# Optimization experiments

Measured on AMD Instinct MI355X. Metric: run time of the kernel, lower is better.

Reference implementation:

```python
import jax, jax.numpy as jnp
import numpy as np
from jax import lax

B, T, D, L, OUT, HORIZON, TSLOTS, NDAY = 512, 24, 1024, 2, 325, 12, 288, 7


def setup_inputs() -> dict:
    key = jax.random.key(0)
    ks = jax.random.split(key, 20)
    s_d = 1.0 / np.sqrt(D)
    s_o = 1.0 / np.sqrt(OUT)
    inp = {
        'data': jax.random.normal(ks[0], (B, T, OUT), jnp.float32),
        'time': jax.random.randint(ks[1], (B, T), 0, TSLOTS),
        'weekday': jax.random.randint(ks[2], (B,), 0, NDAY),
        # embedding params
        'w_data': jax.random.normal(ks[3], (OUT, D), jnp.float32) * s_o,
        'b_data': jnp.zeros((D,), jnp.float32),
        'time_table': jax.random.normal(ks[4], (TSLOTS, D), jnp.float32) * 0.02,
        'day_table': jax.random.normal(ks[5], (NDAY, D), jnp.float32) * 0.02,
        # encoder GRU (input_size == hidden_size == D for all layers)
        'enc_Wih': jax.random.uniform(ks[6], (L, 3 * D, D), jnp.float32, -s_d, s_d),
        'enc_Whh': jax.random.uniform(ks[7], (L, 3 * D, D), jnp.float32, -s_d, s_d),
        'enc_bih': jax.random.uniform(ks[8], (L, 3 * D), jnp.float32, -s_d, s_d),
        'enc_bhh': jax.random.uniform(ks[9], (L, 3 * D), jnp.float32, -s_d, s_d),
        # decoder GRU
        'dec_Wih': jax.random.uniform(ks[10], (L, 3 * D, D), jnp.float32, -s_d, s_d),
        'dec_Whh': jax.random.uniform(ks[11], (L, 3 * D, D), jnp.float32, -s_d, s_d),
        'dec_bih': jax.random.uniform(ks[12], (L, 3 * D), jnp.float32, -s_d, s_d),
        'dec_bhh': jax.random.uniform(ks[13], (L, 3 * D), jnp.float32, -s_d, s_d),
        # decoder output MLP (dropout=0 -> linear)
        'w_mlp': jax.random.uniform(ks[14], (D, OUT), jnp.float32, -s_d, s_d),
        'b_mlp': jnp.zeros((OUT,), jnp.float32),
    }
    return inp


def _gru_cell(h, x, Wih, Whh, bih, bhh):
    # torch GRUCell math. h,x: [B,D]
    gx = x @ Wih.T + bih            # [B,3D]
    gh = h @ Whh.T + bhh
    xr, xz, xn = jnp.split(gx, 3, axis=-1)
    hr, hz, hn = jnp.split(gh, 3, axis=-1)
    r = jax.nn.sigmoid(xr + hr)
    z = jax.nn.sigmoid(xz + hz)
    n = jnp.tanh(xn + r * hn)
    return (1.0 - z) * n + z * h


def _gru_layer(x, h0, Wih, Whh, bih, bhh):
    # x: [B,S,D] -> outputs [B,S,D], final h [B,D]
    def step(h, xt):
        h2 = _gru_cell(h, xt, Wih, Whh, bih, bhh)
        return h2, h2
    hT, ys = lax.scan(step, h0, jnp.moveaxis(x, 1, 0))
    return jnp.moveaxis(ys, 0, 1), hT


def reference(data, time, weekday, w_data, b_data, time_table, day_table,
              enc_Wih, enc_Whh, enc_bih, enc_bhh,
              dec_Wih, dec_Whh, dec_bih, dec_bhh, w_mlp, b_mlp):
    def embed(d, t, wd):  # d:[B,S,OUT] t:[B,S] wd:[B]
        return (d @ w_data + b_data
                + time_table[t % TSLOTS]
                + day_table[wd][:, None, :])

    # ---- encoder over history (all but last step) ----
    x = embed(data[:, :-1], time[:, :-1], weekday)  # [B,T-1,D]
    h_layers = []
    for l in range(L):
        x, hl = _gru_layer(x, jnp.zeros((B, D), x.dtype),
                           enc_Wih[l], enc_Whh[l], enc_bih[l], enc_bhh[l])
        h_layers.append(hl)
    hidden = jnp.stack(h_layers)  # [L,B,D]

    def dec_step(carry, _):
        hidden, data_i, time_i = carry  # [L,B,D], [B,1,OUT], [B,1]
        xi = embed(data_i, time_i, weekday)[:, 0]  # [B,D]
        new_h = []
        h_in = xi
        for l in range(L):
            hl = _gru_cell(hidden[l], h_in, dec_Wih[l], dec_Whh[l],
                           dec_bih[l], dec_bhh[l])
            new_h.append(hl)
            h_in = hl
        res = h_in @ w_mlp + b_mlp              # [B,OUT]
        out_i = data_i[:, 0] + res
        data_next = data_i[:, 0] + lax.stop_gradient(res)
        return (jnp.stack(new_h), data_next[:, None], time_i + 1), out_i

    carry0 = (hidden, data[:, -1:], time[:, -1:])
    _, outs = lax.scan(dec_step, carry0, None, length=HORIZON)  # [H,B,OUT]
    return jnp.moveaxis(outs, 0, 1)  # [B,H,OUT]
```

## Files before the change

### kernel.cpp

```cpp
#include <hip/hip_runtime.h>
#include <math.h>

#define B_ 512
#define T_ 24
#define TM1 23
#define D_ 1024
#define OUT_ 325
#define HORIZON_ 12

typedef unsigned short ushort_t;
typedef __attribute__((ext_vector_type(8))) short bf16x8;
typedef __attribute__((ext_vector_type(4))) float f32x4;

#define MFMA16(a, b, c) __builtin_amdgcn_mfma_f32_16x16x32_bf16((a), (b), (c), 0, 0, 0)

__device__ __forceinline__ ushort_t f2b(float f) {
  union { float f; unsigned u; } v; v.f = f;
  unsigned r = (v.u + 0x7fffu + ((v.u >> 16) & 1u)) >> 16;
  return (ushort_t)r;
}
__device__ __forceinline__ float b2f(ushort_t s) {
  union { unsigned u; float f; } v; v.u = ((unsigned)s) << 16;
  return v.f;
}

__device__ __forceinline__ size_t pidx16(int m, int k, int K) {
  return (((size_t)(m >> 4) * (K >> 5) + (k >> 5)) * 64
          + ((m & 15) + (((k >> 3) & 3) << 4))) * 8 + (k & 7);
}

#define GLOAD16(src, dst) \
  __builtin_amdgcn_global_load_lds((const __attribute__((address_space(1))) void*)(src), \
                                   (__attribute__((address_space(3))) void*)(dst), 16, 0, 0)

#define WAITV2() asm volatile("s_waitcnt vmcnt(2)" ::: "memory")
#define WAITV4() asm volatile("s_waitcnt vmcnt(4)" ::: "memory")
#define WAITV0() asm volatile("s_waitcnt vmcnt(0)" ::: "memory")
#define BARRIER_() { __builtin_amdgcn_s_barrier(); __builtin_amdgcn_sched_barrier(0); }

__global__ __launch_bounds__(256) void enc_diag(
    int k,
    const ushort_t* __restrict__ Hp0, const float* __restrict__ Hf0,
    float* __restrict__ Hf0o, ushort_t* __restrict__ Hp0o,
    const ushort_t* __restrict__ Whh0, const float* __restrict__ bhh0,
    const ushort_t* __restrict__ GXbuf, ushort_t* __restrict__ Y0p,
    const ushort_t* __restrict__ Hp1, const float* __restrict__ Hf1,
    float* __restrict__ Hf1o, ushort_t* __restrict__ Hp1o,
    const ushort_t* __restrict__ Wih1, const ushort_t* __restrict__ Whh1,
    const float* __restrict__ bih1, const float* __restrict__ bhh1)
{
  __shared__ ushort_t lds[3][16 * 512];
  const int tid = threadIdx.x, lane = tid & 63, w = tid >> 6;
  const int bid = blockIdx.x;
  const int z = bid >> 9, bx = (bid >> 5) & 15, by = bid & 31;
  const int wm = w >> 1, wn = w & 1;
  const int d = by * 32 + wn * 16 + (lane & 15);

  if (z == 0) {
    if (k >= TM1) return;
    const ushort_t* GXslot = GXbuf + (size_t)k * 512 * 3072;
    ushort_t* Seqp = Y0p + (size_t)k * 512 * 1024;
    f32x4 acc[3] = {};
    auto stage = [&](int buf, int kb) {
      #pragma unroll
      for (int r = 0; r < 2; ++r) {
        int s = w * 2 + r;
        const ushort_t* src;
        if (s < 2) src = Hp0 + ((size_t)(((bx * 32 + s * 16) >> 4) * 32 + kb)) * 512 + lane * 8;
        else { int g = (s - 2) >> 1, hf = (s - 2) & 1;
          src = Whh0 + ((size_t)((g * 64 + by * 2 + hf) * 32 + kb)) * 512 + lane * 8; }
        GLOAD16(src, &lds[buf][s * 512 + lane * 8]);
      }
    };
    stage(0, 0); stage(1, 1);
    for (int kb = 0; kb < 32; ++kb) {
      if (kb < 31) { WAITV2(); } else { WAITV0(); }
      BARRIER_();
      if (kb + 2 < 32) stage((kb + 2) % 3, kb + 2);
      const ushort_t* L = lds[kb % 3];
      bf16x8 a = *(const bf16x8*)(L + wm * 512 + lane * 8);
      #pragma unroll
      for (int g = 0; g < 3; ++g) {
        bf16x8 b = *(const bf16x8*)(L + (2 + g * 2 + wn) * 512 + lane * 8);
        acc[g] = MFMA16(a, b, acc[g]);
      }
    }
    const float bh_r = bhh0[d], bh_z = bhh0[D_ + d], bh_n = bhh0[2 * D_ + d];
    #pragma unroll
    for (int q = 0; q < 4; ++q) {
      int m = bx * 32 + wm * 16 + ((lane >> 4) << 2) + q;
      const ushort_t* gxp = GXslot + (size_t)m * 3072 + d;
      float gx_r = b2f(gxp[0]), gx_z = b2f(gxp[D_]), gx_n = b2f(gxp[2 * D_]);
      float rr = 1.f / (1.f + __expf(-(gx_r + acc[0][q] + bh_r)));
      float zz = 1.f / (1.f + __expf(-(gx_z + acc[1][q] + bh_z)));
      float nn = tanhf(gx_n + rr * (acc[2][q] + bh_n));
      float h = Hf0[(size_t)m * D_ + d];
      float hnew = (1.f - zz) * nn + zz * h;
      Hf0o[(size_t)m * D_ + d] = hnew;
      ushort_t hb = f2b(hnew);
      size_t pi = pidx16(m, d, D_);
      Hp0o[pi] = hb; Seqp[pi] = hb;
    }
  } else {
    if (k < 1) return;
    const ushort_t* Xp_ = Y0p + (size_t)(k - 1) * 512 * 1024;
    f32x4 accx[3] = {}, acch[3] = {};
    auto stage = [&](int buf, int kb) {
      #pragma unroll
      for (int r = 0; r < 4; ++r) {
        int s = w * 4 + r;
        const ushort_t* src;
        if (s < 2) src = Xp_ + ((size_t)(((bx * 32 + s * 16) >> 4) * 32 + kb)) * 512 + lane * 8;
        else if (s < 4) src = Hp1 + ((size_t)(((bx * 32 + (s - 2) * 16) >> 4) * 32 + kb)) * 512 + lane * 8;
        else if (s < 10) { int g = (s - 4) >> 1, hf = (s - 4) & 1;
          src = Wih1 + ((size_t)((g * 64 + by * 2 + hf) * 32 + kb)) * 512 + lane * 8; }
        else { int g = (s - 10) >> 1, hf = (s - 10) & 1;
          src = Whh1 + ((size_t)((g * 64 + by * 2 + hf) * 32 + kb)) * 512 + lane * 8; }
        GLOAD16(src, &lds[buf][s * 512 + lane * 8]);
      }
    };
    stage(0, 0); stage(1, 1);
    for (int kb = 0; kb < 32; ++kb) {
      if (kb < 31) { WAITV4(); } else { WAITV0(); }
      BARRIER_();
      if (kb + 2 < 32) stage((kb + 2) % 3, kb + 2);
      const ushort_t* L = lds[kb % 3];
      bf16x8 ax = *(const bf16x8*)(L + (0 + wm) * 512 + lane * 8);
      bf16x8 ah = *(const bf16x8*)(L + (2 + wm) * 512 + lane * 8);
      #pragma unroll
      for (int g = 0; g < 3; ++g) {
        bf16x8 bxw = *(const bf16x8*)(L + (4 + g * 2 + wn) * 512 + lane * 8);
        bf16x8 bhw = *(const bf16x8*)(L + (10 + g * 2 + wn) * 512 + lane * 8);
        accx[g] = MFMA16(ax, bxw, accx[g]);
        acch[g] = MFMA16(ah, bhw, acch[g]);
      }
    }
    const float bi_r = bih1[d], bi_z = bih1[D_ + d], bi_n = bih1[2 * D_ + d];
    const float bh_r = bhh1[d], bh_z = bhh1[D_ + d], bh_n = bhh1[2 * D_ + d];
    #pragma unroll
    for (int q = 0; q < 4; ++q) {
      int m = bx * 32 + wm * 16 + ((lane >> 4) << 2) + q;
      float rr = 1.f / (1.f + __expf(-(accx[0][q] + bi_r + acch[0][q] + bh_r)));
      float zz = 1.f / (1.f + __expf(-(accx[1][q] + bi_z + acch[1][q] + bh_z)));
      float nn = tanhf(accx[2][q] + bi_n + rr * (acch[2][q] + bh_n));
      float h = Hf1[(size_t)m * D_ + d];
      float hnew = (1.f - zz) * nn + zz * h;
      Hf1o[(size_t)m * D_ + d] = hnew;
      Hp1o[pidx16(m, d, D_)] = f2b(hnew);
    }
  }
}

__global__ __launch_bounds__(256) void dec_cell0(
    const ushort_t* __restrict__ DCp, const ushort_t* __restrict__ Hp,
    const float* __restrict__ Hf,
    const ushort_t* __restrict__ W0dp, const ushort_t* __restrict__ Whh0,
    const float* __restrict__ bhh0,
    const float* __restrict__ CTt, const float* __restrict__ CBd,
    const int* __restrict__ timev, int step,
    float* __restrict__ Hf_out, ushort_t* __restrict__ Hp_out)
{
  __shared__ ushort_t lds[3][8 * 512];
  const int tid = threadIdx.x, lane = tid & 63, w = tid >> 6;
  const int bid = blockIdx.x;
  const int bx = bid >> 5, by = bid & 31;
  const int wm = w >> 1, wn = w & 1;
  const int d = by * 32 + wn * 16 + (lane & 15);
  f32x4 accx[3] = {}, acch[3] = {};
  const int NT = 43;

  auto stage = [&](int buf, int j) {
    #pragma unroll
    for (int r = 0; r < 2; ++r) {
      int s = w * 2 + r;
      const ushort_t* src;
      if (j < 32) {
        if (s < 2) src = Hp + ((size_t)(((bx * 32 + s * 16) >> 4) * 32 + j)) * 512 + lane * 8;
        else { int g = (s - 2) >> 1, hf = (s - 2) & 1;
          src = Whh0 + ((size_t)((g * 64 + by * 2 + hf) * 32 + j)) * 512 + lane * 8; }
      } else {
        int jj = j - 32;
        if (s < 2) src = DCp + ((size_t)(((bx * 32 + s * 16) >> 4) * 11 + jj)) * 512 + lane * 8;
        else { int g = (s - 2) >> 1, hf = (s - 2) & 1;
          src = W0dp + ((size_t)((g * 64 + by * 2 + hf) * 11 + jj)) * 512 + lane * 8; }
      }
      GLOAD16(src, &lds[buf][s * 512 + lane * 8]);
    }
  };

  stage(0, 0); stage(1, 1);
  for (int j = 0; j < NT; ++j) {
    if (j < NT - 1) { WAITV2(); } else { WAITV0(); }
    BARRIER_();
    if (j + 2 < NT) stage((j + 2) % 3, j + 2);
    const ushort_t* L = lds[j % 3];
    bf16x8 a = *(const bf16x8*)(L + wm * 512 + lane * 8);
    if (j < 32) {
      #pragma unroll
      for (int g = 0; g < 3; ++g) {
        bf16x8 b = *(const bf16x8*)(L + (2 + g * 2 + wn) * 512 + lane * 8);
        acch[g] = MFMA16(a, b, acch[g]);
      }
    } else {
      #pragma unroll
      for (int g = 0; g < 3; ++g) {
        bf16x8 b = *(const bf16x8*)(L + (2 + g * 2 + wn) * 512 + lane * 8);
        accx[g] = MFMA16(a, b, accx[g]);
      }
    }
  }

  const float bh_r = bhh0[d], bh_z = bhh0[D_ + d], bh_n = bhh0[2 * D_ + d];
  #pragma unroll
  for (int q = 0; q < 4; ++q) {
    int m = bx * 32 + wm * 16 + ((lane >> 4) << 2) + q;
    int ti = (timev[m * T_ + (T_ - 1)] + step) % 288;
    const float* ctt = CTt + (size_t)ti * 3072;
    const float* cb  = CBd + (size_t)m * 3072;
    float gx_r = accx[0][q] + ctt[d] + cb[d];
    float gx_z = accx[1][q] + ctt[D_ + d] + cb[D_ + d];
    float gx_n = accx[2][q] + ctt[2 * D_ + d] + cb[2 * D_ + d];
    float rr = 1.f / (1.f + __expf(-(gx_r + acch[0][q] + bh_r)));
    float zz = 1.f / (1.f + __expf(-(gx_z + acch[1][q] + bh_z)));
    float nn = tanhf(gx_n + rr * (acch[2][q] + bh_n));
    float h = Hf[(size_t)m * D_ + d];
    float hnew = (1.f - zz) * nn + zz * h;
    Hf_out[(size_t)m * D_ + d] = hnew;
    Hp_out[pidx16(m, d, D_)] = f2b(hnew);
  }
}

__global__ __launch_bounds__(256) void gru_cell32(
    const ushort_t* __restrict__ Xp_, const ushort_t* __restrict__ Hp,
    const float* __restrict__ Hf,
    const ushort_t* __restrict__ Wih_l, const ushort_t* __restrict__ Whh_l,
    const float* __restrict__ bih_l, const float* __restrict__ bhh_l,
    float* __restrict__ Hf_out, ushort_t* __restrict__ Hp_out)
{
  __shared__ ushort_t lds[3][16 * 512];
  const int tid = threadIdx.x, lane = tid & 63, w = tid >> 6;
  const int bid = blockIdx.x;
  const int bx = bid >> 5, by = bid & 31;
  const int wm = w >> 1, wn = w & 1;
  const int d = by * 32 + wn * 16 + (lane & 15);
  f32x4 accx[3] = {}, acch[3] = {};

  auto stage = [&](int buf, int kb) {
    #pragma unroll
    for (int r = 0; r < 4; ++r) {
      int s = w * 4 + r;
      const ushort_t* src;
      if (s < 2) src = Xp_ + ((size_t)(((bx * 32 + s * 16) >> 4) * 32 + kb)) * 512 + lane * 8;
      else if (s < 4) src = Hp + ((size_t)(((bx * 32 + (s - 2) * 16) >> 4) * 32 + kb)) * 512 + lane * 8;
      else if (s < 10) { int g = (s - 4) >> 1, hf = (s - 4) & 1;
        src = Wih_l + ((size_t)((g * 64 + by * 2 + hf) * 32 + kb)) * 512 + lane * 8; }
      else { int g = (s - 10) >> 1, hf = (s - 10) & 1;
        src = Whh_l + ((size_t)((g * 64 + by * 2 + hf) * 32 + kb)) * 512 + lane * 8; }
      GLOAD16(src, &lds[buf][s * 512 + lane * 8]);
    }
  };

  stage(0, 0); stage(1, 1);
  for (int kb = 0; kb < 32; ++kb) {
    if (kb < 31) { WAITV4(); } else { WAITV0(); }
    BARRIER_();
    if (kb + 2 < 32) stage((kb + 2) % 3, kb + 2);
    const ushort_t* L = lds[kb % 3];
    bf16x8 ax = *(const bf16x8*)(L + (0 + wm) * 512 + lane * 8);
    bf16x8 ah = *(const bf16x8*)(L + (2 + wm) * 512 + lane * 8);
    #pragma unroll
    for (int g = 0; g < 3; ++g) {
      bf16x8 bxw = *(const bf16x8*)(L + (4 + g * 2 + wn) * 512 + lane * 8);
      bf16x8 bhw = *(const bf16x8*)(L + (10 + g * 2 + wn) * 512 + lane * 8);
      accx[g] = MFMA16(ax, bxw, accx[g]);
      acch[g] = MFMA16(ah, bhw, acch[g]);
    }
  }

  const float bi_r = bih_l[d], bi_z = bih_l[D_ + d], bi_n = bih_l[2 * D_ + d];
  const float bh_r = bhh_l[d], bh_z = bhh_l[D_ + d], bh_n = bhh_l[2 * D_ + d];
  #pragma unroll
  for (int q = 0; q < 4; ++q) {
    int m = bx * 32 + wm * 16 + ((lane >> 4) << 2) + q;
    float rr = 1.f / (1.f + __expf(-(accx[0][q] + bi_r + acch[0][q] + bh_r)));
    float zz = 1.f / (1.f + __expf(-(accx[1][q] + bi_z + acch[1][q] + bh_z)));
    float nn = tanhf(accx[2][q] + bi_n + rr * (acch[2][q] + bh_n));
    float h = Hf[(size_t)m * D_ + d];
    float hnew = (1.f - zz) * nn + zz * h;
    Hf_out[(size_t)m * D_ + d] = hnew;
    Hp_out[pidx16(m, d, D_)] = f2b(hnew);
  }
}

__global__ __launch_bounds__(256) void gemm_gx0_enc(
    const ushort_t* __restrict__ Ap, const ushort_t* __restrict__ W0p,
    const float* __restrict__ CTt, const float* __restrict__ CBe,
    const int* __restrict__ timev,
    ushort_t* __restrict__ GX)
{
  __shared__ ushort_t lds[2][16 * 512];
  const int tid = threadIdx.x, lane = tid & 63, w = tid >> 6;
  const int bx = blockIdx.x, by = blockIdx.y;
  const int wm = w >> 1, wn = w & 1;
  f32x4 acc[4][4] = {};

  auto stage = [&](int buf, int kb) {
    #pragma unroll
    for (int r = 0; r < 4; ++r) {
      int s = r * 4 + w;
      const ushort_t* src = (s < 8)
          ? Ap  + ((size_t)((bx * 8 + s) * 11 + kb)) * 512 + lane * 8
          : W0p + ((size_t)((by * 8 + (s - 8)) * 11 + kb)) * 512 + lane * 8;
      GLOAD16(src, &lds[buf][s * 512 + lane * 8]);
    }
  };

  stage(0, 0); __syncthreads();
  int cur = 0;
  for (int kb = 0; kb < 11; ++kb) {
    if (kb + 1 < 11) stage(cur ^ 1, kb + 1);
    const ushort_t* L = lds[cur];
    bf16x8 af[4], bf[4];
    #pragma unroll
    for (int f = 0; f < 4; ++f) {
      af[f] = *(const bf16x8*)(L + (wm * 4 + f) * 512 + lane * 8);
      bf[f] = *(const bf16x8*)(L + (8 + wn * 4 + f) * 512 + lane * 8);
    }
    #pragma unroll
    for (int fm = 0; fm < 4; ++fm)
      #pragma unroll
      for (int fn = 0; fn < 4; ++fn)
        acc[fm][fn] = MFMA16(af[fm], bf[fn], acc[fm][fn]);
    __syncthreads(); cur ^= 1;
  }

  float* fl = (float*)&lds[0][0];
  for (int fm = 0; fm < 4; ++fm) {
    #pragma unroll
    for (int q = 0; q < 4; ++q)
      #pragma unroll
      for (int fn = 0; fn < 4; ++fn)
        fl[(wm * 16 + ((lane >> 4) << 2) + q) * 132 + wn * 64 + fn * 16 + (lane & 15)]
            = acc[fm][fn][q];
    __syncthreads();
    #pragma unroll
    for (int it = 0; it < 2; ++it) {
      int idx = it * 256 + tid;
      int ml = idx >> 4, n0 = (idx & 15) * 8;
      int m = bx * 128 + (ml >> 4) * 64 + fm * 16 + (ml & 15);
      int b = m / 23, t = m - b * 23;
      int ti = timev[b * T_ + t] % 288;
      const float* ctt = CTt + (size_t)ti * 3072 + by * 128 + n0;
      const float* cb  = CBe + (size_t)b * 3072 + by * 128 + n0;
      const float* fr  = fl + ml * 132 + n0;
      bf16x8 o;
      #pragma unroll
      for (int j = 0; j < 8; ++j) o[j] = f2b(fr[j] + ctt[j] + cb[j]);
      *(bf16x8*)(GX + ((size_t)t * 512 + b) * 3072 + by * 128 + n0) = o;
    }
    __syncthreads();
  }
}

template<int EPI>
__global__ __launch_bounds__(256) void gemm64(
    const ushort_t* __restrict__ Ap, const ushort_t* __restrict__ Wp, int K32,
    const float* __restrict__ bias, int step,
    ushort_t* __restrict__ outp, float* __restrict__ outf,
    float* __restrict__ dout, ushort_t* __restrict__ DCp)
{
  __shared__ ushort_t lds[2][8 * 512];
  const int tid = threadIdx.x, lane = tid & 63, w = tid >> 6;
  const int bx = blockIdx.x, by = blockIdx.y;
  const int wm = w >> 1, wn = w & 1;
  f32x4 acc[2][2] = {};

  auto stage = [&](int buf, int kb) {
    #pragma unroll
    for (int r = 0; r < 2; ++r) {
      int s = r * 4 + w;
      const ushort_t* src = (s < 4)
          ? Ap + ((size_t)((bx * 4 + s) * K32 + kb)) * 512 + lane * 8
          : Wp + ((size_t)((by * 4 + (s - 4)) * K32 + kb)) * 512 + lane * 8;
      GLOAD16(src, &lds[buf][s * 512 + lane * 8]);
    }
  };

  stage(0, 0); __syncthreads();
  int cur = 0;
  for (int kb = 0; kb < K32; ++kb) {
    if (kb + 1 < K32) stage(cur ^ 1, kb + 1);
    const ushort_t* L = lds[cur];
    bf16x8 af[2], bf[2];
    #pragma unroll
    for (int f = 0; f < 2; ++f) {
      af[f] = *(const bf16x8*)(L + (wm * 2 + f) * 512 + lane * 8);
      bf[f] = *(const bf16x8*)(L + (4 + wn * 2 + f) * 512 + lane * 8);
    }
    #pragma unroll
    for (int fm = 0; fm < 2; ++fm)
      #pragma unroll
      for (int fn = 0; fn < 2; ++fn)
        acc[fm][fn] = MFMA16(af[fm], bf[fn], acc[fm][fn]);
    __syncthreads(); cur ^= 1;
  }

  #pragma unroll
  for (int fm = 0; fm < 2; ++fm) {
    #pragma unroll
    for (int q = 0; q < 4; ++q) {
      int m = bx * 64 + wm * 32 + fm * 16 + ((lane >> 4) << 2) + q;
      #pragma unroll
      for (int fn = 0; fn < 2; ++fn) {
        int n = by * 64 + wn * 32 + fn * 16 + (lane & 15);
        float v = acc[fm][fn][q];
        if (EPI == 0) {
          if (n < 352) outp[pidx16(m, n, 352)] = f2b(v);
        } else if (EPI == 1) {
          outf[(size_t)m * 3072 + n] = v;
        } else {
          if (n < OUT_) {
            v += bias[n] + outf[(size_t)m * OUT_ + n];
            dout[((size_t)m * HORIZON_ + step) * OUT_ + n] = v;
            outf[(size_t)m * OUT_ + n] = v;
            DCp[pidx16(m, n, 352)] = f2b(v);
          }
        }
      }
    }
  }
}

__global__ void build_cb(const float* __restrict__ CT, const float* __restrict__ bih0,
                         const int* __restrict__ weekday, float* __restrict__ CB)
{
  int idx = blockIdx.x * 256 + threadIdx.x;
  if (idx >= 512 * 3072) return;
  int b = idx / 3072, n = idx - b * 3072;
  CB[idx] = CT[(size_t)(288 + weekday[b]) * 3072 + n] + CT[(size_t)295 * 3072 + n] + bih0[n];
}

__global__ void pack_k1024(const float* __restrict__ src, ushort_t* __restrict__ dst,
                           int total, int Mvalid) {
  int stride = gridDim.x * 256;
  for (int i = blockIdx.x * 256 + threadIdx.x; i < total; i += stride) {
    int seg = i >> 6, q = i & 63;
    int m = (seg >> 5) * 16 + (q & 15);
    int k = (seg & 31) * 32 + (q >> 4) * 8;
    bf16x8 o;
    if (m < Mvalid) {
      const float* s = src + (size_t)m * 1024 + k;
      float4 v0 = *(const float4*)s, v1 = *(const float4*)(s + 4);
      o[0] = f2b(v0.x); o[1] = f2b(v0.y); o[2] = f2b(v0.z); o[3] = f2b(v0.w);
      o[4] = f2b(v1.x); o[5] = f2b(v1.y); o[6] = f2b(v1.z); o[7] = f2b(v1.w);
    } else o = bf16x8{0,0,0,0,0,0,0,0};
    *(bf16x8*)(dst + (size_t)i * 8) = o;
  }
}
__global__ void pack_wm(const float* __restrict__ w_mlp, ushort_t* __restrict__ dst) {
  int stride = gridDim.x * 256;
  for (int i = blockIdx.x * 256 + threadIdx.x; i < 384 * 128; i += stride) {
    int seg = i >> 6, q = i & 63;
    int n = (seg >> 5) * 16 + (q & 15);
    int k = (seg & 31) * 32 + (q >> 4) * 8;
    bf16x8 o;
    #pragma unroll
    for (int j = 0; j < 8; ++j)
      o[j] = (n < OUT_) ? f2b(w_mlp[(size_t)(k + j) * OUT_ + n]) : (short)0;
    *(bf16x8*)(dst + (size_t)i * 8) = o;
  }
}
__global__ void pack_ct(const float* __restrict__ time_table, const float* __restrict__ day_table,
                        const float* __restrict__ b_data, ushort_t* __restrict__ dst) {
  int stride = gridDim.x * 256;
  for (int i = blockIdx.x * 256 + threadIdx.x; i < 320 * 128; i += stride) {
    int seg = i >> 6, q = i & 63;
    int r = (seg >> 5) * 16 + (q & 15);
    int k = (seg & 31) * 32 + (q >> 4) * 8;
    const float* s = nullptr;
    if (r < 288) s = time_table + (size_t)r * 1024 + k;
    else if (r < 295) s = day_table + (size_t)(r - 288) * 1024 + k;
    else if (r == 295) s = b_data + k;
    bf16x8 o;
    #pragma unroll
    for (int j = 0; j < 8; ++j) o[j] = s ? f2b(s[j]) : (short)0;
    *(bf16x8*)(dst + (size_t)i * 8) = o;
  }
}
__global__ void pack_ae(const float* __restrict__ data, ushort_t* __restrict__ Ap) {
  int stride = gridDim.x * 256;
  const int total = (11776 / 16) * 11 * 64;
  for (int i = blockIdx.x * 256 + threadIdx.x; i < total; i += stride) {
    int seg = i >> 6, q = i & 63;
    int m = (seg / 11) * 16 + (q & 15);
    int k = (seg % 11) * 32 + (q >> 4) * 8;
    int b = m / TM1, t = m - b * TM1;
    const float* s = data + ((size_t)b * T_ + t) * OUT_;
    bf16x8 o;
    #pragma unroll
    for (int j = 0; j < 8; ++j) {
      int kk = k + j;
      o[j] = (kk < OUT_) ? f2b(s[kk]) : (short)0;
    }
    *(bf16x8*)(Ap + (size_t)i * 8) = o;
  }
}
__global__ void pack_dc(const float* __restrict__ data, ushort_t* __restrict__ DCp,
                        float* __restrict__ DC) {
  int stride = gridDim.x * 256;
  const int total = (512 / 16) * 11 * 64;
  for (int i = blockIdx.x * 256 + threadIdx.x; i < total; i += stride) {
    int seg = i >> 6, q = i & 63;
    int b = (seg / 11) * 16 + (q & 15);
    int k = (seg % 11) * 32 + (q >> 4) * 8;
    const float* s = data + ((size_t)b * T_ + (T_ - 1)) * OUT_;
    bf16x8 o;
    #pragma unroll
    for (int j = 0; j < 8; ++j) {
      int kk = k + j;
      float v = (kk < OUT_) ? s[kk] : 0.f;
      o[j] = f2b(v);
      if (kk < OUT_) DC[(size_t)b * OUT_ + kk] = v;
    }
    *(bf16x8*)(DCp + (size_t)i * 8) = o;
  }
}

extern "C" void kernel_launch(void* const* d_in, const int* in_sizes, int n_in,
                              void* d_out, int out_size, void* d_ws, size_t ws_size,
                              hipStream_t stream) {
  const float* data       = (const float*)d_in[0];
  const int*   timev      = (const int*)  d_in[1];
  const int*   weekday    = (const int*)  d_in[2];
  const float* w_data     = (const float*)d_in[3];
  const float* b_data     = (const float*)d_in[4];
  const float* time_table = (const float*)d_in[5];
  const float* day_table  = (const float*)d_in[6];
  const float* enc_Wih    = (const float*)d_in[7];
  const float* enc_Whh    = (const float*)d_in[8];
  const float* enc_bih    = (const float*)d_in[9];
  const float* enc_bhh    = (const float*)d_in[10];
  const float* dec_Wih    = (const float*)d_in[11];
  const float* dec_Whh    = (const float*)d_in[12];
  const float* dec_bih    = (const float*)d_in[13];
  const float* dec_bhh    = (const float*)d_in[14];
  const float* w_mlp      = (const float*)d_in[15];
  const float* b_mlp      = (const float*)d_in[16];
  float* out = (float*)d_out;

  char* base = (char*)d_ws;
  size_t o = 0;
  auto take = [&](size_t bytes) { void* p = base + o; o = (o + bytes + 511) & ~(size_t)511; return p; };
  const size_t WSZ = (size_t)6144 * 1024 * 2;
  ushort_t* Wih_e = (ushort_t*)take(WSZ);
  ushort_t* Whh_e = (ushort_t*)take(WSZ);
  ushort_t* Wih_d = (ushort_t*)take(WSZ);
  ushort_t* Whh_d = (ushort_t*)take(WSZ);
  ushort_t* WdTk  = (ushort_t*)take((size_t)384 * 1024 * 2);
  ushort_t* WmT   = (ushort_t*)take((size_t)384 * 1024 * 2);
  ushort_t* CTpk  = (ushort_t*)take((size_t)320 * 1024 * 2);
  ushort_t* W0ep  = (ushort_t*)take((size_t)3072 * 352 * 2);
  ushort_t* W0dp  = (ushort_t*)take((size_t)3072 * 352 * 2);
  float*    CTe   = (float*)take((size_t)320 * 3072 * 4);
  float*    CTd   = (float*)take((size_t)320 * 3072 * 4);
  float*    CBe   = (float*)take((size_t)512 * 3072 * 4);
  float*    CBd   = (float*)take((size_t)512 * 3072 * 4);
  ushort_t* Ap    = (ushort_t*)take((size_t)11776 * 352 * 2);
  ushort_t* Xp    = (ushort_t*)take((size_t)23 * 512 * 1024 * 2);
  ushort_t* GXbuf = (ushort_t*)take((size_t)23 * 512 * 3072 * 2);
  ushort_t* DCp   = (ushort_t*)take((size_t)512 * 352 * 2);
  float*    DC    = (float*)take((size_t)512 * OUT_ * 4);
  float*    Hfb   = (float*)take((size_t)4 * 512 * 1024 * 4 + (size_t)4 * 512 * 1024 * 2);
  if (o > ws_size) return;

  float* Hf0[2], *Hf1[2]; ushort_t* Hp0[2], *Hp1[2];
  ushort_t* Hpb = (ushort_t*)(Hfb + (size_t)4 * 512 * 1024);
  for (int p = 0; p < 2; ++p) {
    Hf0[p] = Hfb + (size_t)p * 512 * 1024;
    Hf1[p] = Hfb + (size_t)(2 + p) * 512 * 1024;
    Hp0[p] = Hpb + (size_t)p * 512 * 1024;
    Hp1[p] = Hpb + (size_t)(2 + p) * 512 * 1024;
  }

  const size_t WLAYER = (size_t)3072 * 1024;

  pack_k1024<<<3072, 256, 0, stream>>>(enc_Wih, Wih_e, 6144 * 128, 6144);
  pack_k1024<<<3072, 256, 0, stream>>>(enc_Whh, Whh_e, 6144 * 128, 6144);
  pack_k1024<<<3072, 256, 0, stream>>>(dec_Wih, Wih_d, 6144 * 128, 6144);
  pack_k1024<<<3072, 256, 0, stream>>>(dec_Whh, Whh_d, 6144 * 128, 6144);
  pack_k1024<<<192, 256, 0, stream>>>(w_data, WdTk, 384 * 128, OUT_);
  pack_wm<<<192, 256, 0, stream>>>(w_mlp, WmT);
  pack_ct<<<160, 256, 0, stream>>>(time_table, day_table, b_data, CTpk);
  pack_ae<<<2048, 256, 0, stream>>>(data, Ap);
  pack_dc<<<88, 256, 0, stream>>>(data, DCp, DC);

  gemm64<0><<<dim3(48, 6), 256, 0, stream>>>(Wih_e, WdTk, 32, nullptr, 0, W0ep, nullptr, nullptr, nullptr);
  gemm64<0><<<dim3(48, 6), 256, 0, stream>>>(Wih_d, WdTk, 32, nullptr, 0, W0dp, nullptr, nullptr, nullptr);
  gemm64<1><<<dim3(5, 48), 256, 0, stream>>>(CTpk, Wih_e, 32, nullptr, 0, nullptr, CTe, nullptr, nullptr);
  gemm64<1><<<dim3(5, 48), 256, 0, stream>>>(CTpk, Wih_d, 32, nullptr, 0, nullptr, CTd, nullptr, nullptr);
  build_cb<<<6144, 256, 0, stream>>>(CTe, enc_bih, weekday, CBe);
  build_cb<<<6144, 256, 0, stream>>>(CTd, dec_bih, weekday, CBd);

  gemm_gx0_enc<<<dim3(92, 24), 256, 0, stream>>>(Ap, W0ep, CTe, CBe, timev, GXbuf);

  hipMemsetAsync(Hf0[0], 0, (size_t)512 * 1024 * 4, stream);
  hipMemsetAsync(Hf1[0], 0, (size_t)512 * 1024 * 4, stream);
  hipMemsetAsync(Hp0[0], 0, (size_t)512 * 1024 * 2, stream);
  hipMemsetAsync(Hp1[0], 0, (size_t)512 * 1024 * 2, stream);

  int p0 = 0, p1 = 0;
  for (int k = 0; k <= TM1; ++k) {
    enc_diag<<<1024, 256, 0, stream>>>(k,
        Hp0[p0], Hf0[p0], Hf0[1 - p0], Hp0[1 - p0], Whh_e, enc_bhh, GXbuf, Xp,
        Hp1[p1], Hf1[p1], Hf1[1 - p1], Hp1[1 - p1],
        Wih_e + WLAYER, Whh_e + WLAYER, enc_bih + 3072, enc_bhh + 3072);
    if (k < TM1) p0 ^= 1;
    if (k >= 1)  p1 ^= 1;
  }

  for (int s = 0; s < HORIZON_; ++s) {
    dec_cell0<<<512, 256, 0, stream>>>(
        DCp, Hp0[p0], Hf0[p0], W0dp, Whh_d, dec_bhh, CTd, CBd, timev, s,
        Hf0[1 - p0], Hp0[1 - p0]);
    p0 ^= 1;
    gru_cell32<<<512, 256, 0, stream>>>(
        Hp0[p0], Hp1[p1], Hf1[p1],
        Wih_d + WLAYER, Whh_d + WLAYER, dec_bih + 3072, dec_bhh + 3072,
        Hf1[1 - p1], Hp1[1 - p1]);
    p1 ^= 1;
    gemm64<3><<<dim3(8, 6), 256, 0, stream>>>(
        Hp1[p1], WmT, 32, b_mlp, s, nullptr, DC, out, DCp);
  }
}
```

Measured before the change: 1.561 ms.

## Replace LDS-staged triple-buffered pipeline with direct global fragment loads in GRU kernels

The recurrent GRU kernels (encoder diagonal, decoder cell 0, generic cell) no longer stage A/B tiles through shared memory with global_load_lds, vmcnt waits and barriers. Each wave now loads its own MFMA fragments straight from the pre-packed global layout, with partial unrolling. This drops the barrier and LDS round-trip cost and frees LDS for occupancy. The cost is that fragments shared by waves (A by the two wn waves, B by the two wm waves) are each fetched twice through L1/L2, and latency hiding now depends on compiler scheduling and occupancy instead of explicit prefetch.

```diff
diff --git a/kernel.cpp b/kernel.cpp
--- a/kernel.cpp
+++ b/kernel.cpp
@@ -33,10 +33,9 @@
   __builtin_amdgcn_global_load_lds((const __attribute__((address_space(1))) void*)(src), \
                                    (__attribute__((address_space(3))) void*)(dst), 16, 0, 0)
 
-#define WAITV2() asm volatile("s_waitcnt vmcnt(2)" ::: "memory")
-#define WAITV4() asm volatile("s_waitcnt vmcnt(4)" ::: "memory")
-#define WAITV0() asm volatile("s_waitcnt vmcnt(0)" ::: "memory")
-#define BARRIER_() { __builtin_amdgcn_s_barrier(); __builtin_amdgcn_sched_barrier(0); }
+__device__ __forceinline__ bf16x8 ldfrag(const ushort_t* p) {
+  return *(const bf16x8*)p;
+}
 
 __global__ __launch_bounds__(256) void enc_diag(
     int k,
@@ -49,41 +48,31 @@
     const ushort_t* __restrict__ Wih1, const ushort_t* __restrict__ Whh1,
     const float* __restrict__ bih1, const float* __restrict__ bhh1)
 {
-  __shared__ ushort_t lds[3][16 * 512];
   const int tid = threadIdx.x, lane = tid & 63, w = tid >> 6;
   const int bid = blockIdx.x;
   const int z = bid >> 9, bx = (bid >> 5) & 15, by = bid & 31;
   const int wm = w >> 1, wn = w & 1;
   const int d = by * 32 + wn * 16 + (lane & 15);
+  const int lo = lane * 8;
 
   if (z == 0) {
     if (k >= TM1) return;
     const ushort_t* GXslot = GXbuf + (size_t)k * 512 * 3072;
     ushort_t* Seqp = Y0p + (size_t)k * 512 * 1024;
     f32x4 acc[3] = {};
-    auto stage = [&](int buf, int kb) {
-      #pragma unroll
-      for (int r = 0; r < 2; ++r) {
-        int s = w * 2 + r;
-        const ushort_t* src;
-        if (s < 2) src = Hp0 + ((size_t)(((bx * 32 + s * 16) >> 4) * 32 + kb)) * 512 + lane * 8;
-        else { int g = (s - 2) >> 1, hf = (s - 2) & 1;
-          src = Whh0 + ((size_t)((g * 64 + by * 2 + hf) * 32 + kb)) * 512 + lane * 8; }
-        GLOAD16(src, &lds[buf][s * 512 + lane * 8]);
-      }
-    };
-    stage(0, 0); stage(1, 1);
+    const ushort_t* aP = Hp0 + ((size_t)(bx * 2 + wm) * 32) * 512 + lo;
+    const ushort_t* bP0 = Whh0 + ((size_t)(0 * 64 + by * 2 + wn) * 32) * 512 + lo;
+    const ushort_t* bP1 = Whh0 + ((size_t)(1 * 64 + by * 2 + wn) * 32) * 512 + lo;
+    const ushort_t* bP2 = Whh0 + ((size_t)(2 * 64 + by * 2 + wn) * 32) * 512 + lo;
+    #pragma unroll 4
     for (int kb = 0; kb < 32; ++kb) {
-      if (kb < 31) { WAITV2(); } else { WAITV0(); }
-      BARRIER_();
-      if (kb + 2 < 32) stage((kb + 2) % 3, kb + 2);
-      const ushort_t* L = lds[kb % 3];
-      bf16x8 a = *(const bf16x8*)(L + wm * 512 + lane * 8);
-      #pragma unroll
-      for (int g = 0; g < 3; ++g) {
-        bf16x8 b = *(const bf16x8*)(L + (2 + g * 2 + wn) * 512 + lane * 8);
-        acc[g] = MFMA16(a, b, acc[g]);
-      }
+      bf16x8 a  = ldfrag(aP  + kb * 512);
+      bf16x8 b0 = ldfrag(bP0 + kb * 512);
+      bf16x8 b1 = ldfrag(bP1 + kb * 512);
+      bf16x8 b2 = ldfrag(bP2 + kb * 512);
+      acc[0] = MFMA16(a, b0, acc[0]);
+      acc[1] = MFMA16(a, b1, acc[1]);
+      acc[2] = MFMA16(a, b2, acc[2]);
     }
     const float bh_r = bhh0[d], bh_z = bhh0[D_ + d], bh_n = bhh0[2 * D_ + d];
     #pragma unroll
@@ -105,35 +94,30 @@
     if (k < 1) return;
     const ushort_t* Xp_ = Y0p + (size_t)(k - 1) * 512 * 1024;
     f32x4 accx[3] = {}, acch[3] = {};
-    auto stage = [&](int buf, int kb) {
-      #pragma unroll
-      for (int r = 0; r < 4; ++r) {
-        int s = w * 4 + r;
-        const ushort_t* src;
-        if (s < 2) src = Xp_ + ((size_t)(((bx * 32 + s * 16) >> 4) * 32 + kb)) * 512 + lane * 8;
-        else if (s < 4) src = Hp1 + ((size_t)(((bx * 32 + (s - 2) * 16) >> 4) * 32 + kb)) * 512 + lane * 8;
-        else if (s < 10) { int g = (s - 4) >> 1, hf = (s - 4) & 1;
-          src = Wih1 + ((size_t)((g * 64 + by * 2 + hf) * 32 + kb)) * 512 + lane * 8; }
-        else { int g = (s - 10) >> 1, hf = (s - 10) & 1;
-          src = Whh1 + ((size_t)((g * 64 + by * 2 + hf) * 32 + kb)) * 512 + lane * 8; }
-        GLOAD16(src, &lds[buf][s * 512 + lane * 8]);
-      }
-    };
-    stage(0, 0); stage(1, 1);
+    const ushort_t* axP = Xp_ + ((size_t)(bx * 2 + wm) * 32) * 512 + lo;
+    const ushort_t* ahP = Hp1 + ((size_t)(bx * 2 + wm) * 32) * 512 + lo;
+    const ushort_t* bxP0 = Wih1 + ((size_t)(0 * 64 + by * 2 + wn) * 32) * 512 + lo;
+    const ushort_t* bxP1 = Wih1 + ((size_t)(1 * 64 + by * 2 + wn) * 32) * 512 + lo;
+    const ushort_t* bxP2 = Wih1 + ((size_t)(2 * 64 + by * 2 + wn) * 32) * 512 + lo;
+    const ushort_t* bhP0 = Whh1 + ((size_t)(0 * 64 + by * 2 + wn) * 32) * 512 + lo;
+    const ushort_t* bhP1 = Whh1 + ((size_t)(1 * 64 + by * 2 + wn) * 32) * 512 + lo;
+    const ushort_t* bhP2 = Whh1 + ((size_t)(2 * 64 + by * 2 + wn) * 32) * 512 + lo;
+    #pragma unroll 2
     for (int kb = 0; kb < 32; ++kb) {
-      if (kb < 31) { WAITV4(); } else { WAITV0(); }
-      BARRIER_();
-      if (kb + 2 < 32) stage((kb + 2) % 3, kb + 2);
-      const ushort_t* L = lds[kb % 3];
-      bf16x8 ax = *(const bf16x8*)(L + (0 + wm) * 512 + lane * 8);
-      bf16x8 ah = *(const bf16x8*)(L + (2 + wm) * 512 + lane * 8);
-      #pragma unroll
-      for (int g = 0; g < 3; ++g) {
-        bf16x8 bxw = *(const bf16x8*)(L + (4 + g * 2 + wn) * 512 + lane * 8);
-        bf16x8 bhw = *(const bf16x8*)(L + (10 + g * 2 + wn) * 512 + lane * 8);
-        accx[g] = MFMA16(ax, bxw, accx[g]);
-        acch[g] = MFMA16(ah, bhw, acch[g]);
-      }
+      bf16x8 ax = ldfrag(axP + kb * 512);
+      bf16x8 ah = ldfrag(ahP + kb * 512);
+      bf16x8 x0 = ldfrag(bxP0 + kb * 512);
+      bf16x8 x1 = ldfrag(bxP1 + kb * 512);
+      bf16x8 x2 = ldfrag(bxP2 + kb * 512);
+      bf16x8 h0 = ldfrag(bhP0 + kb * 512);
+      bf16x8 h1 = ldfrag(bhP1 + kb * 512);
+      bf16x8 h2 = ldfrag(bhP2 + kb * 512);
+      accx[0] = MFMA16(ax, x0, accx[0]);
+      acch[0] = MFMA16(ah, h0, acch[0]);
+      accx[1] = MFMA16(ax, x1, accx[1]);
+      acch[1] = MFMA16(ah, h1, acch[1]);
+      accx[2] = MFMA16(ax, x2, accx[2]);
+      acch[2] = MFMA16(ah, h2, acch[2]);
     }
     const float bi_r = bih1[d], bi_z = bih1[D_ + d], bi_n = bih1[2 * D_ + d];
     const float bh_r = bhh1[d], bh_z = bhh1[D_ + d], bh_n = bhh1[2 * D_ + d];
@@ -160,53 +144,44 @@
     const int* __restrict__ timev, int step,
     float* __restrict__ Hf_out, ushort_t* __restrict__ Hp_out)
 {
-  __shared__ ushort_t lds[3][8 * 512];
   const int tid = threadIdx.x, lane = tid & 63, w = tid >> 6;
   const int bid = blockIdx.x;
   const int bx = bid >> 5, by = bid & 31;
   const int wm = w >> 1, wn = w & 1;
   const int d = by * 32 + wn * 16 + (lane & 15);
+  const int lo = lane * 8;
   f32x4 accx[3] = {}, acch[3] = {};
-  const int NT = 43;
-
-  auto stage = [&](int buf, int j) {
-    #pragma unroll
-    for (int r = 0; r < 2; ++r) {
-      int s = w * 2 + r;
-      const ushort_t* src;
-      if (j < 32) {
-        if (s < 2) src = Hp + ((size_t)(((bx * 32 + s * 16) >> 4) * 32 + j)) * 512 + lane * 8;
-        else { int g = (s - 2) >> 1, hf = (s - 2) & 1;
-          src = Whh0 + ((size_t)((g * 64 + by * 2 + hf) * 32 + j)) * 512 + lane * 8; }
-      } else {
-        int jj = j - 32;
-        if (s < 2) src = DCp + ((size_t)(((bx * 32 + s * 16) >> 4) * 11 + jj)) * 512 + lane * 8;
-        else { int g = (s - 2) >> 1, hf = (s - 2) & 1;
-          src = W0dp + ((size_t)((g * 64 + by * 2 + hf) * 11 + jj)) * 512 + lane * 8; }
-      }
-      GLOAD16(src, &lds[buf][s * 512 + lane * 8]);
-    }
-  };
-
-  stage(0, 0); stage(1, 1);
-  for (int j = 0; j < NT; ++j) {
-    if (j < NT - 1) { WAITV2(); } else { WAITV0(); }
-    BARRIER_();
-    if (j + 2 < NT) stage((j + 2) % 3, j + 2);
-    const ushort_t* L = lds[j % 3];
-    bf16x8 a = *(const bf16x8*)(L + wm * 512 + lane * 8);
-    if (j < 32) {
-      #pragma unroll
-      for (int g = 0; g < 3; ++g) {
-        bf16x8 b = *(const bf16x8*)(L + (2 + g * 2 + wn) * 512 + lane * 8);
-        acch[g] = MFMA16(a, b, acch[g]);
-      }
-    } else {
-      #pragma unroll
-      for (int g = 0; g < 3; ++g) {
-        bf16x8 b = *(const bf16x8*)(L + (2 + g * 2 + wn) * 512 + lane * 8);
-        accx[g] = MFMA16(a, b, accx[g]);
-      }
+
+  {
+    const ushort_t* aP = Hp + ((size_t)(bx * 2 + wm) * 32) * 512 + lo;
+    const ushort_t* bP0 = Whh0 + ((size_t)(0 * 64 + by * 2 + wn) * 32) * 512 + lo;
+    const ushort_t* bP1 = Whh0 + ((size_t)(1 * 64 + by * 2 + wn) * 32) * 512 + lo;
+    const ushort_t* bP2 = Whh0 + ((size_t)(2 * 64 + by * 2 + wn) * 32) * 512 + lo;
+    #pragma unroll 4
+    for (int kb = 0; kb < 32; ++kb) {
+      bf16x8 a  = ldfrag(aP  + kb * 512);
+      bf16x8 b0 = ldfrag(bP0 + kb * 512);
+      bf16x8 b1 = ldfrag(bP1 + kb * 512);
+      bf16x8 b2 = ldfrag(bP2 + kb * 512);
+      acch[0] = MFMA16(a, b0, acch[0]);
+      acch[1] = MFMA16(a, b1, acch[1]);
+      acch[2] = MFMA16(a, b2, acch[2]);
+    }
+  }
+  {
+    const ushort_t* aP = DCp + ((size_t)(bx * 2 + wm) * 11) * 512 + lo;
+    const ushort_t* bP0 = W0dp + ((size_t)(0 * 64 + by * 2 + wn) * 11) * 512 + lo;
+    const ushort_t* bP1 = W0dp + ((size_t)(1 * 64 + by * 2 + wn) * 11) * 512 + lo;
+    const ushort_t* bP2 = W0dp + ((size_t)(2 * 64 + by * 2 + wn) * 11) * 512 + lo;
+    #pragma unroll
+    for (int kb = 0; kb < 11; ++kb) {
+      bf16x8 a  = ldfrag(aP  + kb * 512);
+      bf16x8 b0 = ldfrag(bP0 + kb * 512);
+      bf16x8 b1 = ldfrag(bP1 + kb * 512);
+      bf16x8 b2 = ldfrag(bP2 + kb * 512);
+      accx[0] = MFMA16(a, b0, accx[0]);
+      accx[1] = MFMA16(a, b1, accx[1]);
+      accx[2] = MFMA16(a, b2, accx[2]);
     }
   }
 
@@ -237,44 +212,38 @@
     const float* __restrict__ bih_l, const float* __restrict__ bhh_l,
     float* __restrict__ Hf_out, ushort_t* __restrict__ Hp_out)
 {
-  __shared__ ushort_t lds[3][16 * 512];
   const int tid = threadIdx.x, lane = tid & 63, w = tid >> 6;
   const int bid = blockIdx.x;
   const int bx = bid >> 5, by = bid & 31;
   const int wm = w >> 1, wn = w & 1;
   const int d = by * 32 + wn * 16 + (lane & 15);
+  const int lo = lane * 8;
   f32x4 accx[3] = {}, acch[3] = {};
 
-  auto stage = [&](int buf, int kb) {
-    #pragma unroll
-    for (int r = 0; r < 4; ++r) {
-      int s = w * 4 + r;
-      const ushort_t* src;
-      if (s < 2) src = Xp_ + ((size_t)(((bx * 32 + s * 16) >> 4) * 32 + kb)) * 512 + lane * 8;
-      else if (s < 4) src = Hp + ((size_t)(((bx * 32 + (s - 2) * 16) >> 4) * 32 + kb)) * 512 + lane * 8;
-      else if (s < 10) { int g = (s - 4) >> 1, hf = (s - 4) & 1;
-        src = Wih_l + ((size_t)((g * 64 + by * 2 + hf) * 32 + kb)) * 512 + lane * 8; }
-      else { int g = (s - 10) >> 1, hf = (s - 10) & 1;
-        src = Whh_l + ((size_t)((g * 64 + by * 2 + hf) * 32 + kb)) * 512 + lane * 8; }
-      GLOAD16(src, &lds[buf][s * 512 + lane * 8]);
-    }
-  };
-
-  stage(0, 0); stage(1, 1);
+  const ushort_t* axP = Xp_ + ((size_t)(bx * 2 + wm) * 32) * 512 + lo;
+  const ushort_t* ahP = Hp  + ((size_t)(bx * 2 + wm) * 32) * 512 + lo;
+  const ushort_t* bxP0 = Wih_l + ((size_t)(0 * 64 + by * 2 + wn) * 32) * 512 + lo;
+  const ushort_t* bxP1 = Wih_l + ((size_t)(1 * 64 + by * 2 + wn) * 32) * 512 + lo;
+  const ushort_t* bxP2 = Wih_l + ((size_t)(2 * 64 + by * 2 + wn) * 32) * 512 + lo;
+  const ushort_t* bhP0 = Whh_l + ((size_t)(0 * 64 + by * 2 + wn) * 32) * 512 + lo;
+  const ushort_t* bhP1 = Whh_l + ((size_t)(1 * 64 + by * 2 + wn) * 32) * 512 + lo;
+  const ushort_t* bhP2 = Whh_l + ((size_t)(2 * 64 + by * 2 + wn) * 32) * 512 + lo;
+  #pragma unroll 2
   for (int kb = 0; kb < 32; ++kb) {
-    if (kb < 31) { WAITV4(); } else { WAITV0(); }
-    BARRIER_();
-    if (kb + 2 < 32) stage((kb + 2) % 3, kb + 2);
-    const ushort_t* L = lds[kb % 3];
-    bf16x8 ax = *(const bf16x8*)(L + (0 + wm) * 512 + lane * 8);
-    bf16x8 ah = *(const bf16x8*)(L + (2 + wm) * 512 + lane * 8);
-    #pragma unroll
-    for (int g = 0; g < 3; ++g) {
-      bf16x8 bxw = *(const bf16x8*)(L + (4 + g * 2 + wn) * 512 + lane * 8);
-      bf16x8 bhw = *(const bf16x8*)(L + (10 + g * 2 + wn) * 512 + lane * 8);
-      accx[g] = MFMA16(ax, bxw, accx[g]);
-      acch[g] = MFMA16(ah, bhw, acch[g]);
-    }
+    bf16x8 ax = ldfrag(axP + kb * 512);
+    bf16x8 ah = ldfrag(ahP + kb * 512);
+    bf16x8 x0 = ldfrag(bxP0 + kb * 512);
+    bf16x8 x1 = ldfrag(bxP1 + kb * 512);
+    bf16x8 x2 = ldfrag(bxP2 + kb * 512);
+    bf16x8 h0 = ldfrag(bhP0 + kb * 512);
+    bf16x8 h1 = ldfrag(bhP1 + kb * 512);
+    bf16x8 h2 = ldfrag(bhP2 + kb * 512);
+    accx[0] = MFMA16(ax, x0, accx[0]);
+    acch[0] = MFMA16(ah, h0, acch[0]);
+    accx[1] = MFMA16(ax, x1, accx[1]);
+    acch[1] = MFMA16(ah, h1, acch[1]);
+    accx[2] = MFMA16(ax, x2, accx[2]);
+    acch[2] = MFMA16(ah, h2, acch[2]);
   }
 
   const float bi_r = bih_l[d], bi_z = bih_l[D_ + d], bi_n = bih_l[2 * D_ + d];
```

Measured after the change: 1.564 ms. About the same (+0.2%).
